# Performance work log

Measured on AMD Instinct MI355X. Metric: run time of the kernel, lower is better.

Reference implementation:

```python
import jax, jax.numpy as jnp
import numpy as np

MARGIN = 0.3
WARMUP_EPOCHS = 10
K = 5
ALPHA = 2.0
SAME_CAM_NEG_BOOST = 1.2
NEG_INF = jnp.float32(-jnp.inf)
POS_INF = jnp.float32(jnp.inf)


def setup_inputs() -> dict:
    key = jax.random.key(0)
    k1, k2, k3 = jax.random.split(key, 3)
    N, D = 8192, 2048
    feats = jax.random.normal(k1, (N, D), dtype=jnp.float32)
    labels = jax.random.randint(k2, (N,), 0, 256, dtype=jnp.int64)
    camids = jax.random.randint(k3, (N,), 0, 8, dtype=jnp.int64)
    return {"feats": feats, "labels": labels, "camids": camids, "epoch": 20}


def _topk_mean(dist_mat, mask, k, largest):
    # dist_mat [N,N], mask [N,N] bool. Per-row mean of k largest/smallest valid elems.
    if largest:
        work = jnp.where(mask, dist_mat, NEG_INF)
        vals, _ = jax.lax.top_k(work, k)            # [N,k] largest
        fallback = jnp.max(work, axis=1)
    else:
        work = jnp.where(mask, dist_mat, POS_INF)
        vals = -jax.lax.top_k(-work, k)[0]          # [N,k] smallest
        fallback = jnp.min(work, axis=1)
    is_valid = jnp.isfinite(vals)
    safe_sum = jnp.sum(jnp.where(is_valid, vals, 0.0), axis=1)
    counts = jnp.maximum(is_valid.sum(axis=1), 1)
    mean = safe_sum / counts
    return jnp.where(is_valid.any(axis=1), mean, fallback)


def _forward(feats, labels, camids, epoch):
    # (1) L2 normalize
    norm = jnp.linalg.norm(feats, axis=-1, keepdims=True)
    x = feats / jnp.maximum(norm, 1e-12)
    # Euclidean distance matrix [N,N]
    sq = jnp.sum(x * x, axis=1)
    dist2 = sq[:, None] + sq[None, :] - 2.0 * (x @ x.T)
    dist = jnp.sqrt(jnp.maximum(dist2, 1e-12))
    # masks (constants w.r.t. grad)
    N = feats.shape[0]
    eye = jnp.eye(N, dtype=bool)
    same_label = labels[:, None] == labels[None, :]
    same_cam = camids[:, None] == camids[None, :]
    is_pos = same_label & ~eye & ~same_cam   # cross_cam_pos=True
    is_neg = ~same_label & ~eye
    # boosted same-camera negatives
    neg_bias = jnp.where(is_neg & same_cam, SAME_CAM_NEG_BOOST, 1.0)
    dist_neg_sel = dist / jnp.maximum(neg_bias, 1e-6)
    # (2) top-k hard mining
    d_ap = _topk_mean(dist, is_pos, K, largest=True)
    d_an = _topk_mean(dist_neg_sel, is_neg, K, largest=False)
    # (5) hardness-aware weighting (no grad)
    w = jax.lax.stop_gradient(jax.nn.sigmoid(ALPHA * (d_ap - d_an)))
    w = w / jnp.maximum(w.mean(), 1e-12)
    # (3) margin schedule
    if epoch is not None and epoch < WARMUP_EPOCHS:
        per_sample = jax.nn.softplus(-(d_an - d_ap))
    else:
        per_sample = jax.nn.relu(d_ap - d_an + MARGIN)  # MarginRankingLoss, y=1
    loss = jnp.mean(w * per_sample)
    return loss, jax.lax.stop_gradient(d_ap), jax.lax.stop_gradient(d_an)


def reference(feats, labels, camids, epoch):
    return _forward(feats, labels, camids, epoch)
```

## Files before the change

kernel.cpp:

```cpp
#include <hip/hip_runtime.h>
#include <hip/hip_bf16.h>
#include <stdint.h>

typedef float   floatx4  __attribute__((ext_vector_type(4)));
typedef int     intx4    __attribute__((ext_vector_type(4)));
typedef int     intx8    __attribute__((ext_vector_type(8)));
typedef _Float16 halfx8  __attribute__((ext_vector_type(8)));
typedef _Float16 halfx4  __attribute__((ext_vector_type(4)));
typedef _Float16 half2v  __attribute__((ext_vector_type(2)));
typedef short   short2v  __attribute__((ext_vector_type(2)));
typedef unsigned short ushort8 __attribute__((ext_vector_type(8)));

#define NROW 8192
#define NDIM 2048
#define BM 128
#define BKB 128
#define NSTRIP 64
#define NOFF (NSTRIP*(NSTRIP-1)/2)
#define NTILE (NSTRIP*(NSTRIP+1)/2)
#define DT_LD 136
#define KL_SYM 64
#define MERGE_BLOCKS 128

__device__ __forceinline__ void ins_desc(float (&a)[5], float v) {
#pragma unroll
    for (int k = 0; k < 5; ++k) { float hi = fmaxf(a[k], v); float lo = fminf(a[k], v); a[k] = hi; v = lo; }
}
__device__ __forceinline__ void ins_asc(float (&a)[5], float v) {
#pragma unroll
    for (int k = 0; k < 5; ++k) { float lo = fminf(a[k], v); float hi = fmaxf(a[k], v); a[k] = lo; v = hi; }
}

__device__ __forceinline__ int   h2bits(half2v v) { return __builtin_bit_cast(int, v); }
__device__ __forceinline__ half2v bits2h(int v)   { return __builtin_bit_cast(half2v, v); }
__device__ __forceinline__ int bfi(int m, int a, int b) { return (m & a) | (~m & b); }
__device__ __forceinline__ int nzmask16(int v) {
    short2v s = __builtin_bit_cast(short2v, v);
    short2v n = (short2v)(0) - s;
    int o = v | __builtin_bit_cast(int, n);
    short2v m = __builtin_bit_cast(short2v, o) >> 15;
    return __builtin_bit_cast(int, m);
}
__device__ __forceinline__ int nzmask16_small(int v) {
    short2v s = __builtin_bit_cast(short2v, v);
    short2v n = (short2v)(0) - s;
    short2v m = n >> 15;
    return __builtin_bit_cast(int, m);
}
__device__ __forceinline__ void ins_desc2(half2v (&a)[5], half2v v) {
#pragma unroll
    for (int k = 0; k < 5; ++k) {
        half2v hi = __builtin_elementwise_max(a[k], v);
        half2v lo = __builtin_elementwise_min(a[k], v);
        a[k] = hi; v = lo;
    }
}
__device__ __forceinline__ void ins_asc2(half2v (&a)[5], half2v v) {
#pragma unroll
    for (int k = 0; k < 5; ++k) {
        half2v lo = __builtin_elementwise_min(a[k], v);
        half2v hi = __builtin_elementwise_max(a[k], v);
        a[k] = lo; v = hi;
    }
}

__device__ __forceinline__ void load_lds16(const void* g, void* l) {
    __builtin_amdgcn_global_load_lds((__attribute__((address_space(1))) void*)(void*)g,
                                     (__attribute__((address_space(3))) void*)l,
                                     16, 0, 0);
}

__global__ __launch_bounds__(256) void k_normalize(const float* __restrict__ feats,
                                                   unsigned char* __restrict__ xb,
                                                   float* __restrict__ sq) {
    const int row = blockIdx.x;
    const int t = threadIdx.x;
    const float* f = feats + (size_t)row * NDIM + t * 8;
    float4 v0 = *(const float4*)(f);
    float4 v1 = *(const float4*)(f + 4);
    float ss = v0.x*v0.x + v0.y*v0.y + v0.z*v0.z + v0.w*v0.w
             + v1.x*v1.x + v1.y*v1.y + v1.z*v1.z + v1.w*v1.w;
#pragma unroll
    for (int o = 32; o > 0; o >>= 1) ss += __shfl_down(ss, o);
    __shared__ float red[4];
    __shared__ float s_inv;
    if ((t & 63) == 0) red[t >> 6] = ss;
    __syncthreads();
    if (t == 0) {
        float tot = red[0] + red[1] + red[2] + red[3];
        float m = fmaxf(sqrtf(tot), 1e-12f);
        float inv = 1.0f / m;
        sq[row] = tot * inv * inv;
        s_inv = inv;
    }
    __syncthreads();
    float inv = s_inv;
    int w0 = __builtin_amdgcn_cvt_pk_fp8_f32(v0.x * inv, v0.y * inv, 0, false);
    w0     = __builtin_amdgcn_cvt_pk_fp8_f32(v0.z * inv, v0.w * inv, w0, true);
    int w1 = __builtin_amdgcn_cvt_pk_fp8_f32(v1.x * inv, v1.y * inv, 0, false);
    w1     = __builtin_amdgcn_cvt_pk_fp8_f32(v1.z * inv, v1.w * inv, w1, true);
    int2 pk; pk.x = w0; pk.y = w1;
    *(int2*)(xb + (size_t)row * NDIM + t * 8) = pk;
}

__device__ __forceinline__ void scan_half_row(const _Float16* Dt_,
        const unsigned short* labcam_cols,
        int srow, int shalf, int pli, float (&pos5)[5], float (&neg5)[5]) {
    const int jb = shalf * 64;
    const int s2 = 2 * (srow & 7);
    const int pli2 = pli * 0x00010001;
    const int ONE2  = 0x3C003C00;
    const int BOOST2= 0x398E398E;
    const int PINF2 = 0x7C007C00;
    const int NINF2 = 0xFC00FC00;
    half2v p5[5], n5[5];
#pragma unroll
    for (int k = 0; k < 5; ++k) { p5[k] = bits2h(NINF2); n5[k] = bits2h(PINF2); }
#pragma unroll
    for (int c8 = 0; c8 < 8; ++c8) {
        const int pc = ((shalf * 8 + c8) + s2) & 15;
        intx4 v  = *(const intx4*)(Dt_ + srow * DT_LD + pc * 8);
        intx4 lc = *(const intx4*)(labcam_cols + jb + c8 * 8);
#pragma unroll
        for (int e = 0; e < 4; ++e) {
            const int d2p = v[e];
            const int x   = pli2 ^ lc[e];
            const int mdl = nzmask16(x & 0xFFF0FFF0);
            const int mdc = nzmask16_small(x & 0x000F000F);
            const int mul = bfi(mdc, ONE2, BOOST2);
            half2v nv = bits2h(d2p) * bits2h(mul);
            nv = bits2h(bfi(mdl, h2bits(nv), PINF2));
            ins_asc2(n5, nv);
            const int pmask = mdc & ~mdl;
            half2v pv = bits2h(bfi(pmask, d2p, NINF2));
            half2v chk = __builtin_elementwise_max(pv, p5[4]);
            if (h2bits(chk) != h2bits(p5[4])) ins_desc2(p5, pv);
        }
    }
    half2v tp[5], tn[5];
#pragma unroll
    for (int k = 0; k < 5; ++k) {
        tp[k] = bits2h((int)__builtin_amdgcn_alignbit((unsigned)h2bits(p5[k]), (unsigned)h2bits(p5[k]), 16));
        tn[k] = bits2h((int)__builtin_amdgcn_alignbit((unsigned)h2bits(n5[k]), (unsigned)h2bits(n5[k]), 16));
    }
#pragma unroll
    for (int k = 0; k < 5; ++k) { ins_desc2(p5, tp[k]); ins_asc2(n5, tn[k]); }
#pragma unroll
    for (int k = 0; k < 5; ++k) { pos5[k] = (float)p5[k][0]; neg5[k] = (float)n5[k][0]; }
}

__device__ __forceinline__ void emit_lists(float (&pos5)[5], float (&neg5)[5], int shalf,
        _Float16* posp, _Float16* negp, size_t gi, int slot) {
    float tp[5], tn[5];
#pragma unroll
    for (int k = 0; k < 5; ++k) { tp[k] = __shfl_xor(pos5[k], 1); tn[k] = __shfl_xor(neg5[k], 1); }
#pragma unroll
    for (int k = 0; k < 5; ++k) {
        if (tp[k] > pos5[4]) ins_desc(pos5, tp[k]);
        if (tn[k] < neg5[4]) ins_asc(neg5, tn[k]);
    }
    if (shalf == 0) {
        _Float16* pp = posp + (gi * KL_SYM + slot) * 5;
        _Float16* np = negp + (gi * KL_SYM + slot) * 5;
#pragma unroll
        for (int k = 0; k < 5; ++k) { pp[k] = (_Float16)pos5[k]; np[k] = (_Float16)neg5[k]; }
    }
}

__global__ __launch_bounds__(256, 3) void k_gemm_sym(
        const unsigned char* __restrict__ xb, const float* __restrict__ sq,
        const int* __restrict__ labels, const int* __restrict__ camids,
        _Float16* __restrict__ posp, _Float16* __restrict__ negp) {
    __shared__ __align__(16) char smem[BM * DT_LD * 2 + 4 * BM * 4];
    char* As = smem;
    char* Bs = smem + BM * BKB;
    _Float16* Dt = (_Float16*)smem;
    float* sqr_s = (float*)(smem + BM * DT_LD * 2);
    float* sqc_s = sqr_s + BM;
    unsigned short* labcam_a = (unsigned short*)(sqc_s + BM);
    unsigned short* labcam_b = labcam_a + BM;

    const int tid = threadIdx.x;
    const int w = tid >> 6, lane = tid & 63;
    const int wm = w >> 1, wn = w & 1;

    int a, b;
    {
        int bx = blockIdx.x;
        if (bx < NOFF) {
            a = (int)((1.0f + sqrtf(8.0f * (float)bx + 1.0f)) * 0.5f);
            while (a * (a - 1) / 2 > bx) --a;
            while (a * (a + 1) / 2 <= bx) ++a;
            b = bx - a * (a - 1) / 2;
        } else {
            a = b = bx - NOFF;
        }
    }
    const int r0 = a * BM, c0 = b * BM;

    if (tid < BM) {
        int gi = r0 + tid;
        sqr_s[tid] = sq[gi];
        labcam_a[tid] = (unsigned short)((labels[gi] << 4) | camids[gi]);
    } else {
        int t2 = tid - BM;
        int gj = c0 + t2;
        sqc_s[t2] = sq[gj];
        labcam_b[t2] = (unsigned short)((labels[gj] << 4) | camids[gj]);
    }
    __syncthreads();

    const int srow = tid >> 1;
    const int shalf = tid & 1;

    const int lr = lane >> 3;
    const int lc = ((lane & 7) ^ lr) * 16;
    const int m16 = lane & 15;
    const int quad = lane >> 4;
    const int s7 = m16 & 7;
    const int pc0 = ((2 * quad) ^ s7) * 16;
    const int pc1 = ((2 * quad + 1) ^ s7) * 16;

    floatx4 acc[4][4];
#pragma unroll
    for (int mi = 0; mi < 4; ++mi)
#pragma unroll
        for (int ni = 0; ni < 4; ++ni) {
            floatx4 z = {0.f, 0.f, 0.f, 0.f};
            acc[mi][ni] = z;
        }

    for (int kk = 0; kk < NDIM; kk += BKB) {
        __syncthreads();
#pragma unroll
        for (int q = 0; q < 4; ++q) {
            const int ra = w * 32 + q * 8;
            load_lds16(xb + (size_t)(r0 + ra + lr) * NDIM + kk + lc, As + ra * BKB);
            load_lds16(xb + (size_t)(c0 + ra + lr) * NDIM + kk + lc, Bs + ra * BKB);
        }
        __syncthreads();
        intx8 bfr[4];
#pragma unroll
        for (int ni = 0; ni < 4; ++ni) {
            const char* bp = Bs + (wn * 64 + ni * 16 + m16) * BKB;
            intx4 lo = *(const intx4*)(bp + pc0);
            intx4 hi = *(const intx4*)(bp + pc1);
            bfr[ni] = __builtin_shufflevector(lo, hi, 0, 1, 2, 3, 4, 5, 6, 7);
        }
#pragma unroll
        for (int mi = 0; mi < 4; ++mi) {
            const char* ap = As + (wm * 64 + mi * 16 + m16) * BKB;
            intx4 lo = *(const intx4*)(ap + pc0);
            intx4 hi = *(const intx4*)(ap + pc1);
            intx8 af = __builtin_shufflevector(lo, hi, 0, 1, 2, 3, 4, 5, 6, 7);
#pragma unroll
            for (int ni = 0; ni < 4; ++ni)
                acc[mi][ni] = __builtin_amdgcn_mfma_scale_f32_16x16x128_f8f6f4(
                    af, bfr[ni], acc[mi][ni], 0, 0, 0, 127, 0, 127);
        }
    }
    __syncthreads();

#pragma unroll
    for (int mi = 0; mi < 4; ++mi) {
        const int il = wm * 64 + mi * 16 + quad * 4;
#pragma unroll
        for (int ni = 0; ni < 4; ++ni) {
            const int jl = wn * 64 + ni * 16 + m16;
            const float sj = sqc_s[jl];
#pragma unroll
            for (int r = 0; r < 4; ++r) {
                float d2 = fmaxf(sqr_s[il + r] + sj - 2.0f * acc[mi][ni][r], 1e-12f);
                const int pch = (((jl >> 3) + 2 * ((il + r) & 7)) & 15);
                Dt[(il + r) * DT_LD + (pch << 3) + (jl & 7)] = (_Float16)d2;
            }
        }
    }
    __syncthreads();

    float pos5[5], neg5[5];
    scan_half_row(Dt, labcam_b, srow, shalf, (int)labcam_a[srow], pos5, neg5);
    emit_lists(pos5, neg5, shalf, posp, negp, (size_t)(r0 + srow), b);

    if (a != b) {
        __syncthreads();
#pragma unroll
        for (int ni = 0; ni < 4; ++ni) {
            const int jl = wn * 64 + ni * 16 + m16;
            const float sj = sqc_s[jl];
            const int cw2 = 2 * (jl & 7);
#pragma unroll
            for (int mi = 0; mi < 4; ++mi) {
                const int il = wm * 64 + mi * 16 + quad * 4;
                halfx4 h;
#pragma unroll
                for (int r = 0; r < 4; ++r)
                    h[r] = (_Float16)fmaxf(sqr_s[il + r] + sj - 2.0f * acc[mi][ni][r], 1e-12f);
                const int pch = (((il >> 3) + cw2) & 15);
                *(halfx4*)(Dt + jl * DT_LD + (pch << 3) + (il & 7)) = h;
            }
        }
        __syncthreads();
        scan_half_row(Dt, labcam_a, srow, shalf, (int)labcam_b[srow], pos5, neg5);
        emit_lists(pos5, neg5, shalf, posp, negp, (size_t)(c0 + srow), a);
    }
}

__global__ __launch_bounds__(256) void k_merge_sym(const _Float16* __restrict__ posp,
        const _Float16* __restrict__ negp, const int* __restrict__ epoch_p,
        float* __restrict__ out, float* __restrict__ wsum_p, float* __restrict__ wpsum_p) {
    const int t = threadIdx.x;
    const int rq = t & 3;
    const int row = blockIdx.x * 64 + (t >> 2);
    const float NINF = -__builtin_inff(), PINF = __builtin_inff();
    float p5[5] = {NINF, NINF, NINF, NINF, NINF};
    float n5[5] = {PINF, PINF, PINF, PINF, PINF};
    const halfx8* pv8 = (const halfx8*)(posp + (size_t)row * (KL_SYM * 5) + rq * 80);
    const halfx8* nv8 = (const halfx8*)(negp + (size_t)row * (KL_SYM * 5) + rq * 80);
#pragma unroll
    for (int k = 0; k < 10; ++k) {
        halfx8 v = pv8[k];
#pragma unroll
        for (int e = 0; e < 8; ++e) { float f = (float)v[e]; if (f > p5[4]) ins_desc(p5, f); }
    }
#pragma unroll
    for (int k = 0; k < 10; ++k) {
        halfx8 v = nv8[k];
#pragma unroll
        for (int e = 0; e < 8; ++e) { float f = (float)v[e]; if (f < n5[4]) ins_asc(n5, f); }
    }
#pragma unroll
    for (int o = 1; o <= 2; o <<= 1) {
        float tp[5], tn[5];
#pragma unroll
        for (int k = 0; k < 5; ++k) { tp[k] = __shfl_xor(p5[k], o); tn[k] = __shfl_xor(n5[k], o); }
#pragma unroll
        for (int k = 0; k < 5; ++k) {
            if (tp[k] > p5[4]) ins_desc(p5, tp[k]);
            if (tn[k] < n5[4]) ins_asc(n5, tn[k]);
        }
    }
    float s = 0.f; int c = 0;
#pragma unroll
    for (int k = 0; k < 5; ++k) { bool fin = (p5[k] > NINF); s += fin ? sqrtf(p5[k]) : 0.f; c += fin ? 1 : 0; }
    float d_ap = (c > 0) ? s / (float)c : NINF;
    s = 0.f; c = 0;
#pragma unroll
    for (int k = 0; k < 5; ++k) { bool fin = (n5[k] < PINF); s += fin ? sqrtf(n5[k]) : 0.f; c += fin ? 1 : 0; }
    float d_an = (c > 0) ? s / (float)c : PINF;

    float w0 = 0.f, wp = 0.f;
    if (rq == 0) {
        out[1 + row] = d_ap;
        out[1 + NROW + row] = d_an;
        float diff = d_ap - d_an;
        w0 = 1.0f / (1.0f + expf(-2.0f * diff));
        float p;
        if (*epoch_p < 10) {
            p = fmaxf(diff, 0.0f) + log1pf(expf(-fabsf(diff)));
        } else {
            p = fmaxf(diff + 0.3f, 0.0f);
        }
        wp = w0 * p;
    }
#pragma unroll
    for (int o = 32; o > 0; o >>= 1) { w0 += __shfl_down(w0, o); wp += __shfl_down(wp, o); }
    __shared__ float rw[4], rp[4];
    if ((t & 63) == 0) { rw[t >> 6] = w0; rp[t >> 6] = wp; }
    __syncthreads();
    if (t == 0) {
        wsum_p[blockIdx.x]  = rw[0] + rw[1] + rw[2] + rw[3];
        wpsum_p[blockIdx.x] = rp[0] + rp[1] + rp[2] + rp[3];
    }
}

__global__ void k_finalize(const float* __restrict__ wsum_p, const float* __restrict__ wpsum_p,
                           float* __restrict__ out) {
    const int t = threadIdx.x;
    float sw  = wsum_p[t]  + wsum_p[t + 64];
    float swp = wpsum_p[t] + wpsum_p[t + 64];
#pragma unroll
    for (int o = 32; o > 0; o >>= 1) { sw += __shfl_down(sw, o); swp += __shfl_down(swp, o); }
    if (t == 0) {
        float M = fmaxf(sw / (float)NROW, 1e-12f);
        out[0] = swp / ((float)NROW * M);
    }
}

extern "C" void kernel_launch(void* const* d_in, const int* in_sizes, int n_in,
                              void* d_out, int out_size, void* d_ws, size_t ws_size,
                              hipStream_t stream) {
    const float* feats  = (const float*)d_in[0];
    const int*   labels = (const int*)d_in[1];
    const int*   camids = (const int*)d_in[2];
    const int*   epoch  = (const int*)d_in[3];
    float* out = (float*)d_out;
    char* ws = (char*)d_ws;

    unsigned char* xb = (unsigned char*)ws;
    float* sq = (float*)(ws + 16777216);
    const size_t HALF_LIST_BYTES = (size_t)NROW * KL_SYM * 5 * 2;
    _Float16* posp = (_Float16*)(ws + 16777216 + 32768);
    _Float16* negp = (_Float16*)(ws + 16777216 + 32768 + HALF_LIST_BYTES);
    float* wsum_p  = (float*)(ws + 16777216 + 32768 + 2 * HALF_LIST_BYTES);
    float* wpsum_p = wsum_p + MERGE_BLOCKS;

    k_normalize<<<NROW, 256, 0, stream>>>(feats, xb, sq);
    k_gemm_sym<<<NTILE, 256, 0, stream>>>(xb, sq, labels, camids, posp, negp);
    k_merge_sym<<<MERGE_BLOCKS, 256, 0, stream>>>(posp, negp, epoch, out, wsum_p, wpsum_p);
    k_finalize<<<1, 64, 0, stream>>>(wsum_p, wpsum_p, out);
}
```

Measured before the change: 243.8 us.

## Double-buffer GEMM K-loop, restructure normalize and merge layouts

The fp8 GEMM K-loop now double-buffers the A/B tiles in 64KB of LDS, issuing the next stage's global-to-LDS loads before computing on the current buffer. It also drops one barrier per iteration and raises MFMA priority with setprio, at the cost of lowering occupancy to 2 blocks per CU. Normalize is reworked to one wave per row with no LDS or block barriers. The partial top-5 lists are stored slot-major as padded 16-byte vectors, and the merge kernel uses 32 rows per block with an LDS two-level reduction, so finalize now sums 256 partials.

```diff
diff --git a/kernel.cpp b/kernel.cpp
--- a/kernel.cpp
+++ b/kernel.cpp
@@ -20,7 +20,8 @@
 #define NTILE (NSTRIP*(NSTRIP+1)/2)
 #define DT_LD 136
 #define KL_SYM 64
-#define MERGE_BLOCKS 128
+#define SLOT_P 8
+#define MERGE_BLOCKS 256
 
 __device__ __forceinline__ void ins_desc(float (&a)[5], float v) {
 #pragma unroll
@@ -73,34 +74,27 @@
 __global__ __launch_bounds__(256) void k_normalize(const float* __restrict__ feats,
                                                    unsigned char* __restrict__ xb,
                                                    float* __restrict__ sq) {
-    const int row = blockIdx.x;
-    const int t = threadIdx.x;
-    const float* f = feats + (size_t)row * NDIM + t * 8;
-    float4 v0 = *(const float4*)(f);
-    float4 v1 = *(const float4*)(f + 4);
-    float ss = v0.x*v0.x + v0.y*v0.y + v0.z*v0.z + v0.w*v0.w
-             + v1.x*v1.x + v1.y*v1.y + v1.z*v1.z + v1.w*v1.w;
-#pragma unroll
-    for (int o = 32; o > 0; o >>= 1) ss += __shfl_down(ss, o);
-    __shared__ float red[4];
-    __shared__ float s_inv;
-    if ((t & 63) == 0) red[t >> 6] = ss;
-    __syncthreads();
-    if (t == 0) {
-        float tot = red[0] + red[1] + red[2] + red[3];
-        float m = fmaxf(sqrtf(tot), 1e-12f);
-        float inv = 1.0f / m;
-        sq[row] = tot * inv * inv;
-        s_inv = inv;
-    }
-    __syncthreads();
-    float inv = s_inv;
-    int w0 = __builtin_amdgcn_cvt_pk_fp8_f32(v0.x * inv, v0.y * inv, 0, false);
-    w0     = __builtin_amdgcn_cvt_pk_fp8_f32(v0.z * inv, v0.w * inv, w0, true);
-    int w1 = __builtin_amdgcn_cvt_pk_fp8_f32(v1.x * inv, v1.y * inv, 0, false);
-    w1     = __builtin_amdgcn_cvt_pk_fp8_f32(v1.z * inv, v1.w * inv, w1, true);
-    int2 pk; pk.x = w0; pk.y = w1;
-    *(int2*)(xb + (size_t)row * NDIM + t * 8) = pk;
+    const int lane = threadIdx.x & 63;
+    const int row = (blockIdx.x << 2) + (threadIdx.x >> 6);
+    const float* f = feats + (size_t)row * NDIM;
+    float4 v[8];
+    float ss = 0.f;
+#pragma unroll
+    for (int i = 0; i < 8; ++i) {
+        v[i] = *(const float4*)(f + ((i << 6) + lane) * 4);
+        ss += v[i].x * v[i].x + v[i].y * v[i].y + v[i].z * v[i].z + v[i].w * v[i].w;
+    }
+#pragma unroll
+    for (int o = 32; o > 0; o >>= 1) ss += __shfl_xor(ss, o);
+    float inv = 1.0f / fmaxf(sqrtf(ss), 1e-12f);
+    if (lane == 0) sq[row] = ss * inv * inv;
+    unsigned char* xo = xb + (size_t)row * NDIM;
+#pragma unroll
+    for (int i = 0; i < 8; ++i) {
+        int w0 = __builtin_amdgcn_cvt_pk_fp8_f32(v[i].x * inv, v[i].y * inv, 0, false);
+        w0     = __builtin_amdgcn_cvt_pk_fp8_f32(v[i].z * inv, v[i].w * inv, w0, true);
+        *(int*)(xo + ((i << 6) + lane) * 4) = w0;
+    }
 }
 
 __device__ __forceinline__ void scan_half_row(const _Float16* Dt_,
@@ -150,7 +144,7 @@
 }
 
 __device__ __forceinline__ void emit_lists(float (&pos5)[5], float (&neg5)[5], int shalf,
-        _Float16* posp, _Float16* negp, size_t gi, int slot) {
+        _Float16* posp, _Float16* negp, int gi, int slot) {
     float tp[5], tn[5];
 #pragma unroll
     for (int k = 0; k < 5; ++k) { tp[k] = __shfl_xor(pos5[k], 1); tn[k] = __shfl_xor(neg5[k], 1); }
@@ -160,22 +154,25 @@
         if (tn[k] < neg5[4]) ins_asc(neg5, tn[k]);
     }
     if (shalf == 0) {
-        _Float16* pp = posp + (gi * KL_SYM + slot) * 5;
-        _Float16* np = negp + (gi * KL_SYM + slot) * 5;
-#pragma unroll
-        for (int k = 0; k < 5; ++k) { pp[k] = (_Float16)pos5[k]; np[k] = (_Float16)neg5[k]; }
-    }
-}
-
-__global__ __launch_bounds__(256, 3) void k_gemm_sym(
+        const float NINF = -__builtin_inff(), PINF = __builtin_inff();
+        halfx8 hp, hn;
+#pragma unroll
+        for (int k = 0; k < 5; ++k) { hp[k] = (_Float16)pos5[k]; hn[k] = (_Float16)neg5[k]; }
+        hp[5] = hp[6] = hp[7] = (_Float16)NINF;
+        hn[5] = hn[6] = hn[7] = (_Float16)PINF;
+        const size_t off = ((size_t)slot * NROW + gi) * SLOT_P;
+        *(halfx8*)(posp + off) = hp;
+        *(halfx8*)(negp + off) = hn;
+    }
+}
+
+__global__ __launch_bounds__(256, 2) void k_gemm_sym(
         const unsigned char* __restrict__ xb, const float* __restrict__ sq,
         const int* __restrict__ labels, const int* __restrict__ camids,
         _Float16* __restrict__ posp, _Float16* __restrict__ negp) {
-    __shared__ __align__(16) char smem[BM * DT_LD * 2 + 4 * BM * 4];
-    char* As = smem;
-    char* Bs = smem + BM * BKB;
+    __shared__ __align__(16) char smem[65536 + 2048];
     _Float16* Dt = (_Float16*)smem;
-    float* sqr_s = (float*)(smem + BM * DT_LD * 2);
+    float* sqr_s = (float*)(smem + 65536);
     float* sqc_s = sqr_s + BM;
     unsigned short* labcam_a = (unsigned short*)(sqc_s + BM);
     unsigned short* labcam_b = labcam_a + BM;
@@ -198,6 +195,22 @@
     }
     const int r0 = a * BM, c0 = b * BM;
 
+    const int lr = lane >> 3;
+    const int lc = ((lane & 7) ^ lr) * 16;
+
+    auto stage = [&](int buf, int kkv) {
+        char* Asb = smem + (buf << 15);
+        char* Bsb = Asb + 16384;
+#pragma unroll
+        for (int q = 0; q < 4; ++q) {
+            const int ra = w * 32 + q * 8;
+            load_lds16(xb + (size_t)(r0 + ra + lr) * NDIM + kkv + lc, Asb + ra * BKB);
+            load_lds16(xb + (size_t)(c0 + ra + lr) * NDIM + kkv + lc, Bsb + ra * BKB);
+        }
+    };
+
+    stage(0, 0);
+
     if (tid < BM) {
         int gi = r0 + tid;
         sqr_s[tid] = sq[gi];
@@ -208,13 +221,10 @@
         sqc_s[t2] = sq[gj];
         labcam_b[t2] = (unsigned short)((labels[gj] << 4) | camids[gj]);
     }
-    __syncthreads();
 
     const int srow = tid >> 1;
     const int shalf = tid & 1;
 
-    const int lr = lane >> 3;
-    const int lc = ((lane & 7) ^ lr) * 16;
     const int m16 = lane & 15;
     const int quad = lane >> 4;
     const int s7 = m16 & 7;
@@ -230,26 +240,25 @@
             acc[mi][ni] = z;
         }
 
-    for (int kk = 0; kk < NDIM; kk += BKB) {
-        __syncthreads();
-#pragma unroll
-        for (int q = 0; q < 4; ++q) {
-            const int ra = w * 32 + q * 8;
-            load_lds16(xb + (size_t)(r0 + ra + lr) * NDIM + kk + lc, As + ra * BKB);
-            load_lds16(xb + (size_t)(c0 + ra + lr) * NDIM + kk + lc, Bs + ra * BKB);
-        }
-        __syncthreads();
+    __syncthreads();
+
+    for (int t = 0; t < 16; ++t) {
+        const int cur = t & 1;
+        if (t < 15) stage(cur ^ 1, (t + 1) * BKB);
+        const char* Ab = smem + (cur << 15);
+        const char* Bb = Ab + 16384;
         intx8 bfr[4];
 #pragma unroll
         for (int ni = 0; ni < 4; ++ni) {
-            const char* bp = Bs + (wn * 64 + ni * 16 + m16) * BKB;
+            const char* bp = Bb + (wn * 64 + ni * 16 + m16) * BKB;
             intx4 lo = *(const intx4*)(bp + pc0);
             intx4 hi = *(const intx4*)(bp + pc1);
             bfr[ni] = __builtin_shufflevector(lo, hi, 0, 1, 2, 3, 4, 5, 6, 7);
         }
+        __builtin_amdgcn_s_setprio(1);
 #pragma unroll
         for (int mi = 0; mi < 4; ++mi) {
-            const char* ap = As + (wm * 64 + mi * 16 + m16) * BKB;
+            const char* ap = Ab + (wm * 64 + mi * 16 + m16) * BKB;
             intx4 lo = *(const intx4*)(ap + pc0);
             intx4 hi = *(const intx4*)(ap + pc1);
             intx8 af = __builtin_shufflevector(lo, hi, 0, 1, 2, 3, 4, 5, 6, 7);
@@ -258,8 +267,9 @@
                 acc[mi][ni] = __builtin_amdgcn_mfma_scale_f32_16x16x128_f8f6f4(
                     af, bfr[ni], acc[mi][ni], 0, 0, 0, 127, 0, 127);
         }
-    }
-    __syncthreads();
+        __builtin_amdgcn_s_setprio(0);
+        __syncthreads();
+    }
 
 #pragma unroll
     for (int mi = 0; mi < 4; ++mi) {
@@ -280,7 +290,7 @@
 
     float pos5[5], neg5[5];
     scan_half_row(Dt, labcam_b, srow, shalf, (int)labcam_a[srow], pos5, neg5);
-    emit_lists(pos5, neg5, shalf, posp, negp, (size_t)(r0 + srow), b);
+    emit_lists(pos5, neg5, shalf, posp, negp, r0 + srow, b);
 
     if (a != b) {
         __syncthreads();
@@ -302,7 +312,7 @@
         }
         __syncthreads();
         scan_half_row(Dt, labcam_a, srow, shalf, (int)labcam_b[srow], pos5, neg5);
-        emit_lists(pos5, neg5, shalf, posp, negp, (size_t)(c0 + srow), a);
+        emit_lists(pos5, neg5, shalf, posp, negp, c0 + srow, a);
     }
 }
 
@@ -310,75 +320,80 @@
         const _Float16* __restrict__ negp, const int* __restrict__ epoch_p,
         float* __restrict__ out, float* __restrict__ wsum_p, float* __restrict__ wpsum_p) {
     const int t = threadIdx.x;
-    const int rq = t & 3;
-    const int row = blockIdx.x * 64 + (t >> 2);
+    const int rl = t & 31;
+    const int sg = t >> 5;
+    const int row = blockIdx.x * 32 + rl;
     const float NINF = -__builtin_inff(), PINF = __builtin_inff();
     float p5[5] = {NINF, NINF, NINF, NINF, NINF};
     float n5[5] = {PINF, PINF, PINF, PINF, PINF};
-    const halfx8* pv8 = (const halfx8*)(posp + (size_t)row * (KL_SYM * 5) + rq * 80);
-    const halfx8* nv8 = (const halfx8*)(negp + (size_t)row * (KL_SYM * 5) + rq * 80);
-#pragma unroll
-    for (int k = 0; k < 10; ++k) {
-        halfx8 v = pv8[k];
-#pragma unroll
-        for (int e = 0; e < 8; ++e) { float f = (float)v[e]; if (f > p5[4]) ins_desc(p5, f); }
-    }
-#pragma unroll
-    for (int k = 0; k < 10; ++k) {
-        halfx8 v = nv8[k];
-#pragma unroll
-        for (int e = 0; e < 8; ++e) { float f = (float)v[e]; if (f < n5[4]) ins_asc(n5, f); }
-    }
-#pragma unroll
-    for (int o = 1; o <= 2; o <<= 1) {
-        float tp[5], tn[5];
-#pragma unroll
-        for (int k = 0; k < 5; ++k) { tp[k] = __shfl_xor(p5[k], o); tn[k] = __shfl_xor(n5[k], o); }
-#pragma unroll
-        for (int k = 0; k < 5; ++k) {
-            if (tp[k] > p5[4]) ins_desc(p5, tp[k]);
-            if (tn[k] < n5[4]) ins_asc(n5, tn[k]);
-        }
-    }
-    float s = 0.f; int c = 0;
-#pragma unroll
-    for (int k = 0; k < 5; ++k) { bool fin = (p5[k] > NINF); s += fin ? sqrtf(p5[k]) : 0.f; c += fin ? 1 : 0; }
-    float d_ap = (c > 0) ? s / (float)c : NINF;
-    s = 0.f; c = 0;
-#pragma unroll
-    for (int k = 0; k < 5; ++k) { bool fin = (n5[k] < PINF); s += fin ? sqrtf(n5[k]) : 0.f; c += fin ? 1 : 0; }
-    float d_an = (c > 0) ? s / (float)c : PINF;
-
-    float w0 = 0.f, wp = 0.f;
-    if (rq == 0) {
-        out[1 + row] = d_ap;
-        out[1 + NROW + row] = d_an;
+    const size_t rbase = (size_t)row * SLOT_P;
+#pragma unroll
+    for (int s = 0; s < 8; ++s) {
+        const size_t off = (size_t)(sg * 8 + s) * ((size_t)NROW * SLOT_P) + rbase;
+        halfx8 pv = *(const halfx8*)(posp + off);
+        halfx8 nv = *(const halfx8*)(negp + off);
+#pragma unroll
+        for (int e = 0; e < 8; ++e) { float f = (float)pv[e]; if (f > p5[4]) ins_desc(p5, f); }
+#pragma unroll
+        for (int e = 0; e < 8; ++e) { float f = (float)nv[e]; if (f < n5[4]) ins_asc(n5, f); }
+    }
+    __shared__ __align__(16) _Float16 lp[32][8][8];
+    __shared__ __align__(16) _Float16 ln[32][8][8];
+    const int sw = (sg + rl) & 7;
+    {
+        halfx8 hp, hn;
+#pragma unroll
+        for (int k = 0; k < 5; ++k) { hp[k] = (_Float16)p5[k]; hn[k] = (_Float16)n5[k]; }
+        hp[5] = hp[6] = hp[7] = (_Float16)NINF;
+        hn[5] = hn[6] = hn[7] = (_Float16)PINF;
+        *(halfx8*)&lp[rl][sw][0] = hp;
+        *(halfx8*)&ln[rl][sw][0] = hn;
+    }
+    __syncthreads();
+    if (t < 32) {
+        float P5[5] = {NINF, NINF, NINF, NINF, NINF};
+        float N5[5] = {PINF, PINF, PINF, PINF, PINF};
+#pragma unroll
+        for (int g = 0; g < 8; ++g) {
+            halfx8 pv = *(const halfx8*)&lp[t][g][0];
+            halfx8 nv = *(const halfx8*)&ln[t][g][0];
+#pragma unroll
+            for (int e = 0; e < 8; ++e) { float f = (float)pv[e]; if (f > P5[4]) ins_desc(P5, f); }
+#pragma unroll
+            for (int e = 0; e < 8; ++e) { float f = (float)nv[e]; if (f < N5[4]) ins_asc(N5, f); }
+        }
+        float s = 0.f; int c = 0;
+#pragma unroll
+        for (int k = 0; k < 5; ++k) { bool fin = (P5[k] > NINF); s += fin ? sqrtf(P5[k]) : 0.f; c += fin ? 1 : 0; }
+        float d_ap = (c > 0) ? s / (float)c : NINF;
+        s = 0.f; c = 0;
+#pragma unroll
+        for (int k = 0; k < 5; ++k) { bool fin = (N5[k] < PINF); s += fin ? sqrtf(N5[k]) : 0.f; c += fin ? 1 : 0; }
+        float d_an = (c > 0) ? s / (float)c : PINF;
+
+        const int orow = blockIdx.x * 32 + t;
+        out[1 + orow] = d_ap;
+        out[1 + NROW + orow] = d_an;
         float diff = d_ap - d_an;
-        w0 = 1.0f / (1.0f + expf(-2.0f * diff));
+        float w0 = 1.0f / (1.0f + expf(-2.0f * diff));
         float p;
         if (*epoch_p < 10) {
             p = fmaxf(diff, 0.0f) + log1pf(expf(-fabsf(diff)));
         } else {
             p = fmaxf(diff + 0.3f, 0.0f);
         }
-        wp = w0 * p;
-    }
-#pragma unroll
-    for (int o = 32; o > 0; o >>= 1) { w0 += __shfl_down(w0, o); wp += __shfl_down(wp, o); }
-    __shared__ float rw[4], rp[4];
-    if ((t & 63) == 0) { rw[t >> 6] = w0; rp[t >> 6] = wp; }
-    __syncthreads();
-    if (t == 0) {
-        wsum_p[blockIdx.x]  = rw[0] + rw[1] + rw[2] + rw[3];
-        wpsum_p[blockIdx.x] = rp[0] + rp[1] + rp[2] + rp[3];
+        float wp = w0 * p;
+#pragma unroll
+        for (int o = 16; o > 0; o >>= 1) { w0 += __shfl_down(w0, o, 32); wp += __shfl_down(wp, o, 32); }
+        if (t == 0) { wsum_p[blockIdx.x] = w0; wpsum_p[blockIdx.x] = wp; }
     }
 }
 
 __global__ void k_finalize(const float* __restrict__ wsum_p, const float* __restrict__ wpsum_p,
                            float* __restrict__ out) {
     const int t = threadIdx.x;
-    float sw  = wsum_p[t]  + wsum_p[t + 64];
-    float swp = wpsum_p[t] + wpsum_p[t + 64];
+    float sw  = wsum_p[t] + wsum_p[t + 64] + wsum_p[t + 128] + wsum_p[t + 192];
+    float swp = wpsum_p[t] + wpsum_p[t + 64] + wpsum_p[t + 128] + wpsum_p[t + 192];
 #pragma unroll
     for (int o = 32; o > 0; o >>= 1) { sw += __shfl_down(sw, o); swp += __shfl_down(swp, o); }
     if (t == 0) {
@@ -399,13 +414,13 @@
 
     unsigned char* xb = (unsigned char*)ws;
     float* sq = (float*)(ws + 16777216);
-    const size_t HALF_LIST_BYTES = (size_t)NROW * KL_SYM * 5 * 2;
+    const size_t LIST_HALVES = (size_t)KL_SYM * NROW * SLOT_P;
     _Float16* posp = (_Float16*)(ws + 16777216 + 32768);
-    _Float16* negp = (_Float16*)(ws + 16777216 + 32768 + HALF_LIST_BYTES);
-    float* wsum_p  = (float*)(ws + 16777216 + 32768 + 2 * HALF_LIST_BYTES);
+    _Float16* negp = posp + LIST_HALVES;
+    float* wsum_p  = (float*)((char*)(posp + 2 * LIST_HALVES));
     float* wpsum_p = wsum_p + MERGE_BLOCKS;
 
-    k_normalize<<<NROW, 256, 0, stream>>>(feats, xb, sq);
+    k_normalize<<<NROW / 4, 256, 0, stream>>>(feats, xb, sq);
     k_gemm_sym<<<NTILE, 256, 0, stream>>>(xb, sq, labels, camids, posp, negp);
     k_merge_sym<<<MERGE_BLOCKS, 256, 0, stream>>>(posp, negp, epoch, out, wsum_p, wpsum_p);
     k_finalize<<<1, 64, 0, stream>>>(wsum_p, wpsum_p, out);
```

Measured after the change: 242.8 us. No clear change (-0.4%).
